# Kernel optimization log

Hardware: AMD Instinct MI355X
Metric: run time of the kernel (lower is better)

The kernel has to match this reference:

```python
import jax, jax.numpy as jnp
import numpy as np

HEADS = 16
DIM_HEAD = 64
WINDOW = 16
TOPK_RATIO = 0.1
SCALE = DIM_HEAD ** -0.5


def setup_inputs() -> dict:
    key = jax.random.key(0)
    k1, k2, k3 = jax.random.split(key, 3)
    b, n, d = 2, 2048, 1024
    inner = HEADS * DIM_HEAD
    x = jax.random.normal(k1, (b, n, d), dtype=jnp.float32)
    W_qkv = jax.random.normal(k2, (d, 3 * inner), dtype=jnp.float32) * (d ** -0.5)
    W_out = jax.random.normal(k3, (inner, d), dtype=jnp.float32) * (inner ** -0.5)
    b_out = jnp.zeros((d,), dtype=jnp.float32)
    mask = jnp.ones((b, n), dtype=bool)
    return {"x": x, "W_qkv": W_qkv, "W_out": W_out, "b_out": b_out, "mask": mask}


def reference(x, W_qkv, W_out, b_out, mask):
    b, n, d = x.shape
    h, dh = HEADS, DIM_HEAD
    qkv = x @ W_qkv  # [b, n, 3*h*dh]
    q, k, v = jnp.split(qkv, 3, axis=-1)
    # [b, n, h, dh] -> [b, h, n, dh]
    q = q.reshape(b, n, h, dh).transpose(0, 2, 1, 3)
    k = k.reshape(b, n, h, dh).transpose(0, 2, 1, 3)
    v = v.reshape(b, n, h, dh).transpose(0, 2, 1, 3)

    dots = jnp.einsum('bhid,bhjd->bhij', q, k) * SCALE  # [b, h, n, n]
    NEG = -jnp.finfo(dots.dtype).max

    # sliding window mask: |i - j| <= WINDOW
    idx = jnp.arange(n)
    win = jnp.abs(idx[:, None] - idx[None, :]) <= WINDOW  # [n, n]
    dots = jnp.where(win[None, None], dots, NEG)

    # key padding mask [b, 1, 1, n]
    dots = jnp.where(mask[:, None, None, :], dots, NEG)

    # top-k masking (threshold from kth largest masked score)
    k_value = max(1, int(n * TOPK_RATIO))
    thr = jax.lax.top_k(dots, k_value)[0][..., -1:]  # [b, h, n, 1]
    dots = jnp.where(dots >= thr, dots, NEG)

    attn = jax.nn.softmax(dots, axis=-1)
    out = jnp.einsum('bhij,bhjd->bhid', attn, v)  # [b, h, n, dh]
    out = out.transpose(0, 2, 1, 3).reshape(b, n, h * dh)
    return out @ W_out + b_out
```

## Files before the change

### kernel.cpp

```cpp
#include <hip/hip_runtime.h>
#include <hip/hip_bf16.h>
#include <cstdint>
#include <cstddef>


typedef __hip_bfloat16 bf16;
typedef __attribute__((ext_vector_type(8))) short bf16x8;
typedef __attribute__((ext_vector_type(4))) float f32x4;

#define MFMA16(a, b, c) __builtin_amdgcn_mfma_f32_16x16x32_bf16((a), (b), (c), 0, 0, 0)

__device__ __forceinline__ unsigned short f2bu(float f) {
  return __bfloat16_as_ushort(__float2bfloat16(f));
}

__device__ __forceinline__ void async16(const void* g, void* lds) {
  __builtin_amdgcn_global_load_lds(
      (const __attribute__((address_space(1))) void*)g,
      (__attribute__((address_space(3))) void*)lds, 16, 0, 0);
}

__global__ __launch_bounds__(256) void prep_fused(const float* __restrict__ x,
                                                  const float* __restrict__ Wqkv,
                                                  const float* __restrict__ Wout,
                                                  bf16* __restrict__ xb,
                                                  bf16* __restrict__ wqkvt,
                                                  bf16* __restrict__ woutt) {
  __shared__ bf16 t[32][33];
  int bx = blockIdx.x, tid = threadIdx.x;
  if (bx < 4096) {
    int idx = (bx * 256 + tid) * 4;
    float4 v = *(const float4*)(x + idx);
    union { bf16 h[4]; uint2 u; } pk;
    pk.h[0] = __float2bfloat16(v.x);
    pk.h[1] = __float2bfloat16(v.y);
    pk.h[2] = __float2bfloat16(v.z);
    pk.h[3] = __float2bfloat16(v.w);
    *(uint2*)(xb + idx) = pk.u;
    return;
  }
  const float* W;
  bf16* Wt;
  int N, n0, k0;
  if (bx < 7168) {
    int L = bx - 4096;
    W = Wqkv; Wt = wqkvt; N = 3072;
    n0 = (L % 96) * 32; k0 = (L / 96) * 32;
  } else {
    int L = bx - 7168;
    W = Wout; Wt = woutt; N = 1024;
    n0 = (L & 31) * 32; k0 = (L >> 5) * 32;
  }
  int tx = tid & 31, ty = tid >> 5;
#pragma unroll
  for (int i = 0; i < 32; i += 8)
    t[ty + i][tx] = __float2bfloat16(W[(size_t)(k0 + ty + i) * N + n0 + tx]);
  __syncthreads();
#pragma unroll
  for (int i = 0; i < 32; i += 8)
    Wt[(size_t)(n0 + ty + i) * 1024 + k0 + tx] = t[tx][ty + i];
}

__global__ __launch_bounds__(256, 3) void gemm1_qkv(const bf16* __restrict__ A,
                                                    const bf16* __restrict__ Bt,
                                                    bf16* __restrict__ qkv) {
  const int K = 1024;
  __shared__ __align__(16) char sA[128 * 128];
  __shared__ __align__(16) char sB[128 * 128];
  __shared__ __align__(16) unsigned short sE[4][32 * 68];
  int L = blockIdx.x, xcd = L & 7, s = L >> 3;
  int by = (xcd >> 1) * 8 + s / 12;
  int bx = (xcd & 1) * 12 + s % 12;
  int row0 = by * 128, col0 = bx * 128;
  int tid = threadIdx.x, wave = tid >> 6, lane = tid & 63;
  int wr = wave >> 1, wc = wave & 1;
  int q = lane >> 4, l16 = lane & 15;
  const bf16* srcA[4];
  const bf16* srcB[4];
#pragma unroll
  for (int p = 0; p < 4; ++p) {
    int off = (wave * 4 + p) * 1024 + lane * 16;
    int r = off >> 7;
    int col = ((((off & 127) >> 4) ^ (r & 7)) << 3);
    srcA[p] = A + (size_t)(row0 + r) * K + col;
    srcB[p] = Bt + (size_t)(col0 + r) * K + col;
  }
  int axor = (l16 & 7) << 4;
  f32x4 acc[4][4] = {};
  for (int k0 = 0; k0 < K; k0 += 64) {
    __syncthreads();
#pragma unroll
    for (int p = 0; p < 4; ++p) {
      int chunk = wave * 4 + p;
      async16(srcA[p] + k0, sA + chunk * 1024);
      async16(srcB[p] + k0, sB + chunk * 1024);
    }
    __syncthreads();
#pragma unroll
    for (int half = 0; half < 2; ++half) {
      bf16x8 af[4], bfr[4];
#pragma unroll
      for (int mi = 0; mi < 4; ++mi)
        af[mi] = *(const bf16x8*)(sA + (wr * 64 + mi * 16 + l16) * 128 +
                                  (((half * 4 + q) << 4) ^ axor));
#pragma unroll
      for (int ni = 0; ni < 4; ++ni)
        bfr[ni] = *(const bf16x8*)(sB + (wc * 64 + ni * 16 + l16) * 128 +
                                   (((half * 4 + q) << 4) ^ axor));
#pragma unroll
      for (int mi = 0; mi < 4; ++mi)
#pragma unroll
        for (int ni = 0; ni < 4; ++ni)
          acc[mi][ni] = MFMA16(af[mi], bfr[ni], acc[mi][ni]);
    }
  }
  const size_t TS = (size_t)2 * 16 * 2048 * 64;
  int c_base = col0 + wc * 64;
  int which = c_base >> 10, h = (c_base & 1023) >> 6;
  int r_base = row0 + wr * 64;
  int b = r_base >> 11, i_base = r_base & 2047;
  bf16* dst = qkv + (size_t)which * TS + (((size_t)(b * 16 + h)) * 2048 + i_base) * 64;
  int lr = lane >> 3, lc = lane & 7;
  unsigned short* ep = sE[wave];
#pragma unroll
  for (int ph = 0; ph < 2; ++ph) {
#pragma unroll
    for (int mi2 = 0; mi2 < 2; ++mi2) {
      int mi = ph * 2 + mi2;
#pragma unroll
      for (int ni = 0; ni < 4; ++ni)
#pragma unroll
        for (int t = 0; t < 4; ++t)
          ep[(mi2 * 16 + q * 4 + t) * 68 + ni * 16 + l16] = f2bu(acc[mi][ni][t]);
    }
#pragma unroll
    for (int pass = 0; pass < 4; ++pass) {
      int rloc = pass * 8 + lr;
      uint4 val = *(const uint4*)&ep[rloc * 68 + lc * 8];
      *(uint4*)(dst + (size_t)(ph * 32 + rloc) * 64 + lc * 8) = val;
    }
  }
}

__global__ __launch_bounds__(256, 3) void gemm2_out(const bf16* __restrict__ A,
                                                    const bf16* __restrict__ Bt,
                                                    const float* __restrict__ bias,
                                                    float* __restrict__ out) {
  const int K = 1024, N = 1024;
  __shared__ __align__(16) char sA[128 * 128];
  __shared__ __align__(16) char sB[64 * 128];
  int L = blockIdx.x, xcd = L & 7, s = L >> 3;
  int by = (xcd >> 1) * 8 + (s >> 3);
  int bx = (xcd & 1) * 8 + (s & 7);
  int row0 = by * 128, col0 = bx * 64;
  int tid = threadIdx.x, wave = tid >> 6, lane = tid & 63;
  int wr = wave >> 1, wc = wave & 1;
  int q = lane >> 4, l16 = lane & 15;
  const bf16* srcA[4];
  const bf16* srcB[2];
#pragma unroll
  for (int p = 0; p < 4; ++p) {
    int off = (wave * 4 + p) * 1024 + lane * 16;
    int r = off >> 7;
    int col = ((((off & 127) >> 4) ^ (r & 7)) << 3);
    srcA[p] = A + (size_t)(row0 + r) * K + col;
  }
#pragma unroll
  for (int p = 0; p < 2; ++p) {
    int off = (wave * 2 + p) * 1024 + lane * 16;
    int r = off >> 7;
    int col = ((((off & 127) >> 4) ^ (r & 7)) << 3);
    srcB[p] = Bt + (size_t)(col0 + r) * K + col;
  }
  int axor = (l16 & 7) << 4;
  f32x4 acc[4][2] = {};
  for (int k0 = 0; k0 < K; k0 += 64) {
    __syncthreads();
#pragma unroll
    for (int p = 0; p < 4; ++p) async16(srcA[p] + k0, sA + (wave * 4 + p) * 1024);
#pragma unroll
    for (int p = 0; p < 2; ++p) async16(srcB[p] + k0, sB + (wave * 2 + p) * 1024);
    __syncthreads();
#pragma unroll
    for (int half = 0; half < 2; ++half) {
      bf16x8 af[4], bfr[2];
#pragma unroll
      for (int mi = 0; mi < 4; ++mi)
        af[mi] = *(const bf16x8*)(sA + (wr * 64 + mi * 16 + l16) * 128 +
                                  (((half * 4 + q) << 4) ^ axor));
#pragma unroll
      for (int ni = 0; ni < 2; ++ni)
        bfr[ni] = *(const bf16x8*)(sB + (wc * 32 + ni * 16 + l16) * 128 +
                                   (((half * 4 + q) << 4) ^ axor));
#pragma unroll
      for (int mi = 0; mi < 4; ++mi)
#pragma unroll
        for (int ni = 0; ni < 2; ++ni)
          acc[mi][ni] = MFMA16(af[mi], bfr[ni], acc[mi][ni]);
    }
  }
#pragma unroll
  for (int mi = 0; mi < 4; ++mi) {
#pragma unroll
    for (int ni = 0; ni < 2; ++ni) {
      int c = col0 + wc * 32 + ni * 16 + l16;
      float bv = bias[c];
#pragma unroll
      for (int t = 0; t < 4; ++t) {
        int r = row0 + wr * 64 + mi * 16 + q * 4 + t;
        out[(size_t)r * N + c] = acc[mi][ni][t] + bv;
      }
    }
  }
}

__global__ __launch_bounds__(256, 4) void attn_mfma(const bf16* __restrict__ qkv,
                                                    bf16* __restrict__ aout) {
  __shared__ __align__(16) unsigned short sQ[64 * 72];
  __shared__ __align__(16) unsigned short sK[96 * 72];
  __shared__ __align__(16) unsigned short sVt[64 * 120];

  int tid = threadIdx.x, wave = tid >> 6, lane = tid & 63;
  int quad = lane >> 4, l16 = lane & 15;
  int bh = blockIdx.x >> 5, qb = blockIdx.x & 31;
  int i0 = qb * 64, jbase = i0 - 16;
  const size_t TS = (size_t)32 * 2048 * 64;
  const bf16* qbase = qkv + (size_t)bh * 2048 * 64;
  const bf16* kbase = qbase + TS;
  const bf16* vbase = qbase + 2 * TS;

#pragma unroll
  for (int u = tid; u < 512; u += 256) {
    int row = u >> 3, cg = u & 7;
    uint4 val = *(const uint4*)(qbase + (size_t)(i0 + row) * 64 + cg * 8);
    *(uint4*)&sQ[row * 72 + cg * 8] = val;
  }
#pragma unroll
  for (int u = tid; u < 768; u += 256) {
    int slot = u >> 3, cg = u & 7;
    int j = jbase + slot;
    uint4 val = make_uint4(0, 0, 0, 0);
    if ((unsigned)j < 2048u) val = *(const uint4*)(kbase + (size_t)j * 64 + cg * 8);
    *(uint4*)&sK[slot * 72 + cg * 8] = val;
  }
#pragma unroll
  for (int u = tid; u < 768; u += 256) {
    int slot = u >> 3, cg = u & 7;
    int j = jbase + slot;
    union { uint4 v; unsigned short s[8]; } pk;
    pk.v = make_uint4(0, 0, 0, 0);
    if ((unsigned)j < 2048u) pk.v = *(const uint4*)(vbase + (size_t)j * 64 + cg * 8);
#pragma unroll
    for (int d = 0; d < 8; ++d) sVt[(cg * 8 + d) * 120 + slot] = pk.s[d];
  }
  {
    int d = tid >> 2, s0 = 96 + (tid & 3) * 4;
    *(uint2*)&sVt[d * 120 + s0] = make_uint2(0, 0);
  }
  __syncthreads();

  int m0 = wave * 16;
  bf16x8 aq[2];
#pragma unroll
  for (int ks = 0; ks < 2; ++ks)
    aq[ks] = *(const bf16x8*)&sQ[(m0 + l16) * 72 + ks * 32 + quad * 8];
  f32x4 s[3] = {};
#pragma unroll
  for (int nt = 0; nt < 3; ++nt)
#pragma unroll
    for (int ks = 0; ks < 2; ++ks) {
      bf16x8 bk = *(const bf16x8*)&sK[(m0 + nt * 16 + l16) * 72 + ks * 32 + quad * 8];
      s[nt] = MFMA16(aq[ks], bk, s[nt]);
    }

  float rinv[4];
#pragma unroll
  for (int t = 0; t < 4; ++t) {
    int r = quad * 4 + t;
    float mx = -INFINITY;
#pragma unroll
    for (int nt = 0; nt < 3; ++nt) {
      int cl = nt * 16 + l16;
      int j = jbase + m0 + cl;
      bool valid = ((unsigned)(cl - r) <= 32u) && ((unsigned)j < 2048u);
      float v = valid ? s[nt][t] * 0.125f : -INFINITY;
      s[nt][t] = v;
      mx = fmaxf(mx, v);
    }
#pragma unroll
    for (int msk = 8; msk; msk >>= 1) mx = fmaxf(mx, __shfl_xor(mx, msk));
    float sum = 0.f;
#pragma unroll
    for (int nt = 0; nt < 3; ++nt) {
      float ev = __expf(s[nt][t] - mx);
      s[nt][t] = ev;
      sum += ev;
    }
#pragma unroll
    for (int msk = 8; msk; msk >>= 1) sum += __shfl_xor(sum, msk);
    rinv[t] = 1.0f / sum;
  }

  unsigned short* sPw = &sQ[m0 * 72];
#pragma unroll
  for (int t = 0; t < 4; ++t) {
#pragma unroll
    for (int nt = 0; nt < 3; ++nt)
      sPw[(quad * 4 + t) * 72 + nt * 16 + l16] = f2bu(s[nt][t]);
    sPw[(quad * 4 + t) * 72 + 48 + l16] = 0;
  }

  bf16x8 ap[2];
#pragma unroll
  for (int ks = 0; ks < 2; ++ks)
    ap[ks] = *(const bf16x8*)&sPw[l16 * 72 + ks * 32 + quad * 8];
  f32x4 o[4] = {};
#pragma unroll
  for (int dt = 0; dt < 4; ++dt)
#pragma unroll
    for (int ks = 0; ks < 2; ++ks) {
      bf16x8 bv = *(const bf16x8*)&sVt[(dt * 16 + l16) * 120 + m0 + ks * 32 + quad * 8];
      o[dt] = MFMA16(ap[ks], bv, o[dt]);
    }

  int b = bh >> 4, h = bh & 15;
#pragma unroll
  for (int dt = 0; dt < 4; ++dt)
#pragma unroll
    for (int t = 0; t < 4; ++t) {
      int r = i0 + m0 + quad * 4 + t;
      aout[((size_t)(b * 2048 + r)) * 1024 + h * 64 + dt * 16 + l16] =
          __float2bfloat16(o[dt][t] * rinv[t]);
    }
}

extern "C" void kernel_launch(void* const* d_in, const int* in_sizes, int n_in,
                              void* d_out, int out_size, void* d_ws, size_t ws_size,
                              hipStream_t stream) {
  const float* x = (const float*)d_in[0];
  const float* Wqkv = (const float*)d_in[1];
  const float* Wout = (const float*)d_in[2];
  const float* bout = (const float*)d_in[3];

  char* ws = (char*)d_ws;
  bf16* xb = (bf16*)(ws);
  bf16* wqkvt = (bf16*)(ws + 8388608);
  bf16* woutt = (bf16*)(ws + 14680064);
  bf16* qkvb = (bf16*)(ws + 16777216);
  bf16* aout = xb;

  hipLaunchKernelGGL(prep_fused, dim3(8192), dim3(256), 0, stream, x, Wqkv, Wout, xb, wqkvt, woutt);
  hipLaunchKernelGGL(gemm1_qkv, dim3(768), dim3(256), 0, stream, xb, wqkvt, qkvb);
  hipLaunchKernelGGL(attn_mfma, dim3(1024), dim3(256), 0, stream, qkvb, aout);
  hipLaunchKernelGGL(gemm2_out, dim3(512), dim3(256), 0, stream, aout, woutt, bout,
                     (float*)d_out);
}
```

Before: 140.3 us.

## Pre-pack QKV GEMM operands into MFMA fragment layout and load directly from global

The prep kernel now writes x and W_qkv in a packed 16-row by 8-k fragment layout, so each lane's bf16x8 MFMA operand sits contiguously in memory. The QKV GEMM drops its LDS staging, barriers and swizzle and reads fragments straight from global memory (through cache), unrolling the K loop. This removes LDS traffic and synchronisation but loses cross-wave operand sharing in LDS and relies on L2/L1 for reuse, and the x conversion becomes a heavier transpose-through-LDS pass.

```diff
diff --git a/kernel.cpp b/kernel.cpp
--- a/kernel.cpp
+++ b/kernel.cpp
@@ -23,101 +23,104 @@
 __global__ __launch_bounds__(256) void prep_fused(const float* __restrict__ x,
                                                   const float* __restrict__ Wqkv,
                                                   const float* __restrict__ Wout,
-                                                  bf16* __restrict__ xb,
-                                                  bf16* __restrict__ wqkvt,
+                                                  bf16* __restrict__ xpk,
+                                                  bf16* __restrict__ wqkvpk,
                                                   bf16* __restrict__ woutt) {
+  __shared__ float sT[16][268];
   __shared__ bf16 t[32][33];
   int bx = blockIdx.x, tid = threadIdx.x;
-  if (bx < 4096) {
-    int idx = (bx * 256 + tid) * 4;
-    float4 v = *(const float4*)(x + idx);
-    union { bf16 h[4]; uint2 u; } pk;
-    pk.h[0] = __float2bfloat16(v.x);
-    pk.h[1] = __float2bfloat16(v.y);
-    pk.h[2] = __float2bfloat16(v.z);
-    pk.h[3] = __float2bfloat16(v.w);
-    *(uint2*)(xb + idx) = pk.u;
+  if (bx < 256) {
+    int p = bx;
+    const float* xs = x + (size_t)p * 16 * 1024;
+#pragma unroll
+    for (int ch = 0; ch < 4; ++ch) {
+#pragma unroll
+      for (int i = 0; i < 4; ++i) {
+        int row = (tid >> 6) * 4 + i;
+        int c4 = tid & 63;
+        float4 v = *(const float4*)(xs + (size_t)row * 1024 + ch * 256 + c4 * 4);
+        *(float4*)&sT[row][c4 * 4] = v;
+      }
+      __syncthreads();
+      int r = tid & 15;
+#pragma unroll
+      for (int gg = 0; gg < 2; ++gg) {
+        int g = (tid >> 4) + gg * 16;
+        union { uint4 u; unsigned short h[8]; } pk;
+#pragma unroll
+        for (int j = 0; j < 8; ++j) pk.h[j] = f2bu(sT[r][g * 8 + j]);
+        *(uint4*)(xpk + ((size_t)(p * 128 + ch * 32 + g)) * 128 + r * 8) = pk.u;
+      }
+      __syncthreads();
+    }
     return;
   }
-  const float* W;
-  bf16* Wt;
-  int N, n0, k0;
-  if (bx < 7168) {
-    int L = bx - 4096;
-    W = Wqkv; Wt = wqkvt; N = 3072;
-    n0 = (L % 96) * 32; k0 = (L / 96) * 32;
-  } else {
-    int L = bx - 7168;
-    W = Wout; Wt = woutt; N = 1024;
-    n0 = (L & 31) * 32; k0 = (L >> 5) * 32;
-  }
-  int tx = tid & 31, ty = tid >> 5;
-#pragma unroll
-  for (int i = 0; i < 32; i += 8)
-    t[ty + i][tx] = __float2bfloat16(W[(size_t)(k0 + ty + i) * N + n0 + tx]);
-  __syncthreads();
-#pragma unroll
-  for (int i = 0; i < 32; i += 8)
-    Wt[(size_t)(n0 + ty + i) * 1024 + k0 + tx] = t[tx][ty + i];
-}
-
-__global__ __launch_bounds__(256, 3) void gemm1_qkv(const bf16* __restrict__ A,
-                                                    const bf16* __restrict__ Bt,
+  if (bx < 3328) {
+    int L = bx - 256;
+    int n0 = (L % 96) * 32, k0 = (L / 96) * 32;
+    int tx = tid & 31, ty = tid >> 5;
+#pragma unroll
+    for (int i = 0; i < 32; i += 8)
+      t[ty + i][tx] = __float2bfloat16(Wqkv[(size_t)(k0 + ty + i) * 3072 + n0 + tx]);
+    __syncthreads();
+    int chunk = tid >> 5;
+    int sub = chunk >> 2, g = chunk & 3;
+    int inner = tid & 31;
+    int nn = inner >> 1, kk = (inner & 1) * 4;
+    int n = n0 + sub * 16 + nn, k = k0 + g * 8 + kk;
+    union { uint2 u; unsigned short h[4]; } pk;
+#pragma unroll
+    for (int j = 0; j < 4; ++j)
+      pk.h[j] = __bfloat16_as_ushort(t[g * 8 + kk + j][sub * 16 + nn]);
+    *(uint2*)(wqkvpk + ((size_t)(n >> 4) * 128 + (k >> 3)) * 128 + nn * 8 + kk) = pk.u;
+    return;
+  }
+  {
+    int L = bx - 3328;
+    int n0 = (L & 31) * 32, k0 = (L >> 5) * 32;
+    int tx = tid & 31, ty = tid >> 5;
+#pragma unroll
+    for (int i = 0; i < 32; i += 8)
+      t[ty + i][tx] = __float2bfloat16(Wout[(size_t)(k0 + ty + i) * 1024 + n0 + tx]);
+    __syncthreads();
+#pragma unroll
+    for (int i = 0; i < 32; i += 8)
+      woutt[(size_t)(n0 + ty + i) * 1024 + k0 + tx] = t[tx][ty + i];
+  }
+}
+
+__global__ __launch_bounds__(256, 3) void gemm1_qkv(const bf16* __restrict__ Apk,
+                                                    const bf16* __restrict__ Bpk,
                                                     bf16* __restrict__ qkv) {
-  const int K = 1024;
-  __shared__ __align__(16) char sA[128 * 128];
-  __shared__ __align__(16) char sB[128 * 128];
   __shared__ __align__(16) unsigned short sE[4][32 * 68];
   int L = blockIdx.x, xcd = L & 7, s = L >> 3;
   int by = (xcd >> 1) * 8 + s / 12;
   int bx = (xcd & 1) * 12 + s % 12;
-  int row0 = by * 128, col0 = bx * 128;
+  int col0 = bx * 128;
   int tid = threadIdx.x, wave = tid >> 6, lane = tid & 63;
   int wr = wave >> 1, wc = wave & 1;
   int q = lane >> 4, l16 = lane & 15;
-  const bf16* srcA[4];
-  const bf16* srcB[4];
-#pragma unroll
-  for (int p = 0; p < 4; ++p) {
-    int off = (wave * 4 + p) * 1024 + lane * 16;
-    int r = off >> 7;
-    int col = ((((off & 127) >> 4) ^ (r & 7)) << 3);
-    srcA[p] = A + (size_t)(row0 + r) * K + col;
-    srcB[p] = Bt + (size_t)(col0 + r) * K + col;
-  }
-  int axor = (l16 & 7) << 4;
+  const bf16* pa = Apk + (size_t)(by * 8 + wr * 4) * 16384 + q * 128 + l16 * 8;
+  const bf16* pb = Bpk + (size_t)(bx * 8 + wc * 4) * 16384 + q * 128 + l16 * 8;
   f32x4 acc[4][4] = {};
-  for (int k0 = 0; k0 < K; k0 += 64) {
-    __syncthreads();
-#pragma unroll
-    for (int p = 0; p < 4; ++p) {
-      int chunk = wave * 4 + p;
-      async16(srcA[p] + k0, sA + chunk * 1024);
-      async16(srcB[p] + k0, sB + chunk * 1024);
-    }
-    __syncthreads();
-#pragma unroll
-    for (int half = 0; half < 2; ++half) {
-      bf16x8 af[4], bfr[4];
-#pragma unroll
-      for (int mi = 0; mi < 4; ++mi)
-        af[mi] = *(const bf16x8*)(sA + (wr * 64 + mi * 16 + l16) * 128 +
-                                  (((half * 4 + q) << 4) ^ axor));
+#pragma unroll 4
+  for (int k0 = 0; k0 < 1024; k0 += 32) {
+    int koff = k0 * 16;
+    bf16x8 af[4], bfr[4];
+#pragma unroll
+    for (int mi = 0; mi < 4; ++mi) af[mi] = *(const bf16x8*)(pa + mi * 16384 + koff);
+#pragma unroll
+    for (int ni = 0; ni < 4; ++ni) bfr[ni] = *(const bf16x8*)(pb + ni * 16384 + koff);
+#pragma unroll
+    for (int mi = 0; mi < 4; ++mi)
 #pragma unroll
       for (int ni = 0; ni < 4; ++ni)
-        bfr[ni] = *(const bf16x8*)(sB + (wc * 64 + ni * 16 + l16) * 128 +
-                                   (((half * 4 + q) << 4) ^ axor));
-#pragma unroll
-      for (int mi = 0; mi < 4; ++mi)
-#pragma unroll
-        for (int ni = 0; ni < 4; ++ni)
-          acc[mi][ni] = MFMA16(af[mi], bfr[ni], acc[mi][ni]);
-    }
+        acc[mi][ni] = MFMA16(af[mi], bfr[ni], acc[mi][ni]);
   }
   const size_t TS = (size_t)2 * 16 * 2048 * 64;
   int c_base = col0 + wc * 64;
   int which = c_base >> 10, h = (c_base & 1023) >> 6;
-  int r_base = row0 + wr * 64;
+  int r_base = by * 128 + wr * 64;
   int b = r_base >> 11, i_base = r_base & 2047;
   bf16* dst = qkv + (size_t)which * TS + (((size_t)(b * 16 + h)) * 2048 + i_base) * 64;
   int lr = lane >> 3, lc = lane & 7;
@@ -343,14 +346,15 @@
   const float* bout = (const float*)d_in[3];
 
   char* ws = (char*)d_ws;
-  bf16* xb = (bf16*)(ws);
-  bf16* wqkvt = (bf16*)(ws + 8388608);
+  bf16* xpk = (bf16*)(ws);
+  bf16* wqkvpk = (bf16*)(ws + 8388608);
   bf16* woutt = (bf16*)(ws + 14680064);
   bf16* qkvb = (bf16*)(ws + 16777216);
-  bf16* aout = xb;
-
-  hipLaunchKernelGGL(prep_fused, dim3(8192), dim3(256), 0, stream, x, Wqkv, Wout, xb, wqkvt, woutt);
-  hipLaunchKernelGGL(gemm1_qkv, dim3(768), dim3(256), 0, stream, xb, wqkvt, qkvb);
+  bf16* aout = xpk;
+
+  hipLaunchKernelGGL(prep_fused, dim3(4352), dim3(256), 0, stream, x, Wqkv, Wout,
+                     xpk, wqkvpk, woutt);
+  hipLaunchKernelGGL(gemm1_qkv, dim3(768), dim3(256), 0, stream, xpk, wqkvpk, qkvb);
   hipLaunchKernelGGL(attn_mfma, dim3(1024), dim3(256), 0, stream, qkvb, aout);
   hipLaunchKernelGGL(gemm2_out, dim3(512), dim3(256), 0, stream, aout, woutt, bout,
                      (float*)d_out);
```

After: 143.5 us. 1.02x slower.
